# Optimization experiments

Hardware: AMD Instinct MI355X
Metric: run time of the kernel (lower is better)

The kernel has to match this reference:

```python
import jax, jax.numpy as jnp
import numpy as np

D_IN = 1024
D_OUT = 1024
NUM_HEADS = 16
HEAD_DIM = D_OUT // NUM_HEADS


def setup_inputs() -> dict:
    key = jax.random.key(0)
    ks = jax.random.split(key, 6)
    b, T = 2, 2048
    scale = 0.02
    x = jax.random.normal(ks[0], (b, T, D_IN), dtype=jnp.float32)
    Wq = jax.random.normal(ks[1], (D_IN, D_OUT), dtype=jnp.float32) * scale
    Wk = jax.random.normal(ks[2], (D_IN, D_OUT), dtype=jnp.float32) * scale
    Wv = jax.random.normal(ks[3], (D_IN, D_OUT), dtype=jnp.float32) * scale
    Wo = jax.random.normal(ks[4], (D_OUT, D_OUT), dtype=jnp.float32) * scale
    bo = jnp.zeros((D_OUT,), dtype=jnp.float32)
    return {"x": x, "Wq": Wq, "Wk": Wk, "Wv": Wv, "Wo": Wo, "bo": bo}


def reference(x, Wq, Wk, Wv, Wo, bo):
    b, T, _ = x.shape
    H, Dh = NUM_HEADS, HEAD_DIM
    # projections: [b,T,d_out] -> [b,H,T,Dh]
    q = (x @ Wq).reshape(b, T, H, Dh).transpose(0, 2, 1, 3)
    k = (x @ Wk).reshape(b, T, H, Dh).transpose(0, 2, 1, 3)
    v = (x @ Wv).reshape(b, T, H, Dh).transpose(0, 2, 1, 3)
    # scores: [b,H,T,T]
    att = jnp.einsum('bhqd,bhkd->bhqk', q, k)
    causal = jnp.triu(jnp.ones((T, T), dtype=bool), k=1)
    att = jnp.where(causal, -jnp.inf, att)
    att = jax.nn.softmax(att / np.sqrt(Dh).astype(np.float32), axis=-1)
    # dropout p=0.0 -> identity
    y = jnp.einsum('bhqk,bhkd->bhqd', att, v)
    y = y.transpose(0, 2, 1, 3).reshape(b, T, H * Dh)
    return y @ Wo + bo
```

## Files before the change

### kernel.cpp

```cpp
#include <hip/hip_runtime.h>

#define T_   2048
#define DM   1024
#define H_   16
#define DH   64

typedef unsigned short u16;
typedef unsigned int u32;
typedef __attribute__((ext_vector_type(8))) short bf16x8;
typedef __attribute__((ext_vector_type(8))) unsigned short u16x8;
typedef __attribute__((ext_vector_type(4))) float f32x4;
typedef __attribute__((ext_vector_type(16))) float f32x16;
typedef __attribute__((ext_vector_type(4))) unsigned int u32x4;
typedef __attribute__((ext_vector_type(2))) unsigned int u32x2;

static __device__ __forceinline__ u16 f2b(float f) {
  unsigned int u = __builtin_bit_cast(unsigned int, f);
  u += 0x7fff + ((u >> 16) & 1);
  return (u16)(u >> 16);
}

static __device__ __forceinline__ u32 cvtpk(float a, float b) {
  u32 d;
  asm("v_cvt_pk_bf16_f32 %0, %1, %2" : "=v"(d) : "v"(a), "v"(b));
  return d;
}

static __device__ __forceinline__ void gll16(const void* g, void* l) {
  __builtin_amdgcn_global_load_lds(
      (const __attribute__((address_space(1))) unsigned int*)g,
      (__attribute__((address_space(3))) unsigned int*)l, 16, 0, 0);
}

static __device__ __forceinline__ bf16x8 ldf(const char* base, int rho,
                                             int k16) {
  return *(const bf16x8*)(base + rho * 128 + ((k16 ^ (rho & 7)) << 4));
}


__global__ __launch_bounds__(256) void k_cvt_x(const float* __restrict__ x,
                                               u16* __restrict__ o) {
  int i = (blockIdx.x * 256 + threadIdx.x) * 8;
  float4 a = *(const float4*)(x + i);
  float4 b = *(const float4*)(x + i + 4);
  u16x8 r;
  r[0] = f2b(a.x); r[1] = f2b(a.y); r[2] = f2b(a.z); r[3] = f2b(a.w);
  r[4] = f2b(b.x); r[5] = f2b(b.y); r[6] = f2b(b.z); r[7] = f2b(b.w);
  *(u16x8*)(o + i) = r;
}

__global__ __launch_bounds__(256) void k_cvt_wt(
    const float* __restrict__ Wq, const float* __restrict__ Wk,
    const float* __restrict__ Wv, const float* __restrict__ Wo,
    u16* __restrict__ oq, u16* __restrict__ ok, u16* __restrict__ ov,
    u16* __restrict__ oo) {
  const float* W; u16* Wt;
  int z = blockIdx.z;
  if (z == 0)      { W = Wq; Wt = oq; }
  else if (z == 1) { W = Wk; Wt = ok; }
  else if (z == 2) { W = Wv; Wt = ov; }
  else             { W = Wo; Wt = oo; }
  const float wsc = (z == 0) ? 0.1803368801111204f : 1.0f;
  __shared__ u16 tile[64][65];
  int k0 = blockIdx.x * 64, n0 = blockIdx.y * 64;
  int r = threadIdx.x >> 2, c0 = (threadIdx.x & 3) * 16;
  const float* src = W + (k0 + r) * DM + n0 + c0;
#pragma unroll
  for (int e = 0; e < 16; e += 4) {
    float4 v = *(const float4*)(src + e);
    tile[r][c0 + e + 0] = f2b(v.x * wsc);
    tile[r][c0 + e + 1] = f2b(v.y * wsc);
    tile[r][c0 + e + 2] = f2b(v.z * wsc);
    tile[r][c0 + e + 3] = f2b(v.w * wsc);
  }
  __syncthreads();
  u16x8 a, b;
#pragma unroll
  for (int e = 0; e < 8; ++e) a[e] = tile[c0 + e][r];
#pragma unroll
  for (int e = 0; e < 8; ++e) b[e] = tile[c0 + 8 + e][r];
  u16* dst = Wt + (n0 + r) * DM + k0 + c0;
  *(u16x8*)dst = a;
  *(u16x8*)(dst + 8) = b;
}

__global__ __launch_bounds__(256) void k_qkv(
    const u16* __restrict__ X, const u16* __restrict__ Wqt,
    const u16* __restrict__ Wkt, const u16* __restrict__ Wvt,
    u16* __restrict__ Qg, u16* __restrict__ Kg, u16* __restrict__ Vtg) {
  __shared__ char smem[34816];
  char* As = smem;
  char* Bs = smem + 16384;
  const int tid = threadIdx.x, lane = tid & 63, w = tid >> 6;
  const int frow = lane & 15, fk = lane >> 4;
  const int wr = (w >> 1) * 64, wc = (w & 1) * 64;
  const int m0 = blockIdx.x * 128;
  const int by = blockIdx.y;
  const int z = by >> 3, n0 = (by & 7) * 128;
  const u16* Wt = (z == 0) ? Wqt : (z == 1) ? Wkt : Wvt;
  const u16* Ap = X + m0 * DM;
  const u16* Bp = Wt + n0 * DM;
  const int ro = lane >> 3;
  const int ce = ((lane & 7) ^ ro) << 3;

  f32x4 acc[4][4];
#pragma unroll
  for (int mi = 0; mi < 4; ++mi)
#pragma unroll
    for (int ni = 0; ni < 4; ++ni) acc[mi][ni] = (f32x4){0.f, 0.f, 0.f, 0.f};

  for (int k0 = 0; k0 < DM; k0 += 64) {
#pragma unroll
    for (int c = 0; c < 4; ++c) {
      const int g8 = (w * 4 + c) * 8;
      gll16(Ap + (g8 + ro) * DM + k0 + ce, As + g8 * 128);
      gll16(Bp + (g8 + ro) * DM + k0 + ce, Bs + g8 * 128);
    }
    asm volatile("s_waitcnt vmcnt(0)" ::: "memory");
    __syncthreads();
    bf16x8 a[4][2], b[4][2];
#pragma unroll
    for (int mi = 0; mi < 4; ++mi)
#pragma unroll
      for (int kk = 0; kk < 2; ++kk)
        a[mi][kk] = ldf(As, wr + mi * 16 + frow, kk * 4 + fk);
#pragma unroll
    for (int ni = 0; ni < 4; ++ni)
#pragma unroll
      for (int kk = 0; kk < 2; ++kk)
        b[ni][kk] = ldf(Bs, wc + ni * 16 + frow, kk * 4 + fk);
#pragma unroll
    for (int mi = 0; mi < 4; ++mi)
#pragma unroll
      for (int ni = 0; ni < 4; ++ni)
#pragma unroll
        for (int kk = 0; kk < 2; ++kk)
          acc[mi][ni] = __builtin_amdgcn_mfma_f32_16x16x32_bf16(
              a[mi][kk], b[ni][kk], acc[mi][ni], 0, 0, 0);
    __syncthreads();
  }

  if (z < 2) {
    u16* out = (z == 0) ? Qg : Kg;
#pragma unroll
    for (int mi = 0; mi < 4; ++mi)
#pragma unroll
      for (int ni = 0; ni < 4; ++ni)
#pragma unroll
        for (int r = 0; r < 4; ++r) {
          int m = m0 + wr + mi * 16 + fk * 4 + r;
          int nl = n0 + wc + ni * 16 + frow;
          int b = m >> 11, t = m & 2047, h = nl >> 6, d = nl & 63;
          out[((b * H_ + h) * T_ + t) * DH + d] = f2b(acc[mi][ni][r]);
        }
  } else {
    u16* Tl = (u16*)smem;
#pragma unroll
    for (int ni = 0; ni < 4; ++ni) {
      const int n = wc + ni * 16 + frow;
#pragma unroll
      for (int mi = 0; mi < 4; ++mi)
#pragma unroll
        for (int r = 0; r < 4; ++r)
          Tl[n * 136 + wr + mi * 16 + fk * 4 + r] = f2b(acc[mi][ni][r]);
    }
    __syncthreads();
    const int n = tid >> 1, c0 = (tid & 1) * 64;
    const int ng = n0 + n, h = ng >> 6, d = ng & 63;
    const int b = m0 >> 11;
    const int tb = (m0 & 2047) + c0;
    u16* dst = Vtg + ((b * H_ + h) * DH + d) * T_ + tb;
#pragma unroll
    for (int e = 0; e < 8; ++e)
      *(u16x8*)(dst + e * 8) = *(const u16x8*)(Tl + n * 136 + c0 + e * 8);
  }
}

__global__ __launch_bounds__(256) void k_out(
    const u16* __restrict__ Y, const u16* __restrict__ Wot,
    const float* __restrict__ bo, float* __restrict__ out) {
  __shared__ char smem[24576];
  char* As = smem;
  char* Bs = smem + 8192;
  const int tid = threadIdx.x, lane = tid & 63, w = tid >> 6;
  const int frow = lane & 15, fk = lane >> 4;
  const int wr = (w >> 1) * 32, wc = (w & 1) * 64;
  const int m0 = blockIdx.x * 64, n0 = blockIdx.y * 128;
  const u16* Ap = Y + m0 * DM;
  const u16* Bp = Wot + n0 * DM;
  const int ro = lane >> 3;
  const int ce = ((lane & 7) ^ ro) << 3;

  f32x4 acc[2][4];
#pragma unroll
  for (int mi = 0; mi < 2; ++mi)
#pragma unroll
    for (int ni = 0; ni < 4; ++ni) acc[mi][ni] = (f32x4){0.f, 0.f, 0.f, 0.f};

  for (int k0 = 0; k0 < DM; k0 += 64) {
#pragma unroll
    for (int c = 0; c < 2; ++c) {
      const int g8 = (w * 2 + c) * 8;
      gll16(Ap + (g8 + ro) * DM + k0 + ce, As + g8 * 128);
    }
#pragma unroll
    for (int c = 0; c < 4; ++c) {
      const int g8 = (w * 4 + c) * 8;
      gll16(Bp + (g8 + ro) * DM + k0 + ce, Bs + g8 * 128);
    }
    asm volatile("s_waitcnt vmcnt(0)" ::: "memory");
    __syncthreads();
    bf16x8 a[2][2], b[4][2];
#pragma unroll
    for (int mi = 0; mi < 2; ++mi)
#pragma unroll
      for (int kk = 0; kk < 2; ++kk)
        a[mi][kk] = ldf(As, wr + mi * 16 + frow, kk * 4 + fk);
#pragma unroll
    for (int ni = 0; ni < 4; ++ni)
#pragma unroll
      for (int kk = 0; kk < 2; ++kk)
        b[ni][kk] = ldf(Bs, wc + ni * 16 + frow, kk * 4 + fk);
#pragma unroll
    for (int mi = 0; mi < 2; ++mi)
#pragma unroll
      for (int ni = 0; ni < 4; ++ni)
#pragma unroll
        for (int kk = 0; kk < 2; ++kk)
          acc[mi][ni] = __builtin_amdgcn_mfma_f32_16x16x32_bf16(
              a[mi][kk], b[ni][kk], acc[mi][ni], 0, 0, 0);
    __syncthreads();
  }
#pragma unroll
  for (int mi = 0; mi < 2; ++mi)
#pragma unroll
    for (int ni = 0; ni < 4; ++ni)
#pragma unroll
      for (int r = 0; r < 4; ++r) {
        int m = m0 + wr + mi * 16 + fk * 4 + r;
        int n = n0 + wc + ni * 16 + frow;
        out[m * DM + n] = acc[mi][ni][r] + bo[n];
      }
}

__global__ __launch_bounds__(128) void k_attn(
    const u16* __restrict__ Qg, const u16* __restrict__ Kg,
    const u16* __restrict__ Vtg, u16* __restrict__ Yg) {
  __shared__ char Kl[2][8192];
  __shared__ char Vl[2][8192];
  const int bh = blockIdx.x;
  const int qt = 31 - blockIdx.y;
  const int q0 = qt * 64;
  const int tid = threadIdx.x, w = tid >> 6, lane = tid & 63;
  const int hi = lane >> 5, qq = lane & 31;
  const u16* Qb = Qg + bh * (T_ * DH);
  const u16* Kb = Kg + bh * (T_ * DH);
  const u16* Vb = Vtg + bh * (DH * T_);
  const int qrow = q0 + w * 32 + qq;

  bf16x8 qf[4];
#pragma unroll
  for (int kb = 0; kb < 4; ++kb)
    qf[kb] = *(const bf16x8*)(Qb + qrow * DH + kb * 16 + hi * 8);

  f32x16 o0, o1;
#pragma unroll
  for (int r = 0; r < 16; ++r) { o0[r] = 0.f; o1[r] = 0.f; }
  float m = -1e30f, lp = 0.f;

  const int nt = qt + 1;
  const int ro = lane >> 3;
  const int ce = ((lane & 7) ^ ro) << 3;

#pragma unroll
  for (int c = 0; c < 4; ++c) {
    const int g = w * 4 + c;
    gll16(Kb + (g * 8 + ro) * DH + ce, Kl[0] + g * 1024);
    gll16(Vb + (g * 8 + ro) * T_ + ce, Vl[0] + g * 1024);
  }
  asm volatile("s_waitcnt vmcnt(0)" ::: "memory");
  __syncthreads();

  for (int t = 0; t < nt; ++t) {
    const char* Kc = Kl[t & 1];
    const char* Vc = Vl[t & 1];
    if (t + 1 < nt) {
      const int jn = (t + 1) * 64;
      char* Kn = Kl[(t + 1) & 1];
      char* Vn = Vl[(t + 1) & 1];
#pragma unroll
      for (int c = 0; c < 4; ++c) {
        const int g = w * 4 + c;
        gll16(Kb + (jn + g * 8 + ro) * DH + ce, Kn + g * 1024);
        gll16(Vb + (g * 8 + ro) * T_ + jn + ce, Vn + g * 1024);
      }
    }

    f32x16 s0, s1;
#pragma unroll
    for (int r = 0; r < 16; ++r) { s0[r] = 0.f; s1[r] = 0.f; }
#pragma unroll
    for (int kb = 0; kb < 4; ++kb) {
      bf16x8 ka0 = *(const bf16x8*)(
          Kc + qq * 128 + (((kb * 2 + hi) ^ (qq & 7)) << 4));
      s0 = __builtin_amdgcn_mfma_f32_32x32x16_bf16(ka0, qf[kb], s0, 0, 0, 0);
      bf16x8 ka1 = *(const bf16x8*)(
          Kc + (qq + 32) * 128 + (((kb * 2 + hi) ^ (qq & 7)) << 4));
      s1 = __builtin_amdgcn_mfma_f32_32x32x16_bf16(ka1, qf[kb], s1, 0, 0, 0);
    }
    if (t == nt - 1) {
#pragma unroll
      for (int r = 0; r < 16; ++r) {
        const int cr = q0 + (r & 3) + 8 * (r >> 2) + 4 * hi;
        if (cr > qrow) s0[r] = -1e30f;
        if (cr + 32 > qrow) s1[r] = -1e30f;
      }
    }
    float tm[16];
#pragma unroll
    for (int r = 0; r < 16; ++r) tm[r] = fmaxf(s0[r], s1[r]);
#pragma unroll
    for (int st = 8; st > 0; st >>= 1)
#pragma unroll
      for (int r = 0; r < st; ++r) tm[r] = fmaxf(tm[r], tm[r + st]);
    const float mt = fmaxf(tm[0], __shfl_xor(tm[0], 32));
    if (__any(mt > m + 8.f)) {
      const float mn = fmaxf(m, mt);
      const float al = __builtin_amdgcn_exp2f(m - mn);
      m = mn;
#pragma unroll
      for (int r = 0; r < 16; ++r) { o0[r] *= al; o1[r] *= al; }
      lp *= al;
    }
    float ts[16];
#pragma unroll
    for (int r = 0; r < 16; ++r) {
      s0[r] = __builtin_amdgcn_exp2f(s0[r] - m);
      s1[r] = __builtin_amdgcn_exp2f(s1[r] - m);
      ts[r] = s0[r] + s1[r];
    }
#pragma unroll
    for (int st = 8; st > 0; st >>= 1)
#pragma unroll
      for (int r = 0; r < st; ++r) ts[r] += ts[r + st];
    lp += ts[0];
    bf16x8 pb[4];
#define MKCH(DST, S, RB)                                                     \
  {                                                                          \
    u32 a01 = cvtpk(S[RB + 0], S[RB + 1]);                                   \
    u32 a23 = cvtpk(S[RB + 2], S[RB + 3]);                                   \
    u32 a45 = cvtpk(S[RB + 4], S[RB + 5]);                                   \
    u32 a67 = cvtpk(S[RB + 6], S[RB + 7]);                                   \
    asm volatile("v_permlane32_swap_b32 %0, %1" : "+v"(a01), "+v"(a45));     \
    asm volatile("v_permlane32_swap_b32 %0, %1" : "+v"(a23), "+v"(a67));     \
    u32x4 t4;                                                                \
    t4[0] = a01; t4[1] = a23; t4[2] = a45; t4[3] = a67;                      \
    DST = __builtin_bit_cast(bf16x8, t4);                                    \
  }
    MKCH(pb[0], s0, 0)
    MKCH(pb[1], s0, 8)
    MKCH(pb[2], s1, 0)
    MKCH(pb[3], s1, 8)
#undef MKCH
#pragma unroll
    for (int jc = 0; jc < 4; ++jc) {
      bf16x8 va0 = *(const bf16x8*)(
          Vc + qq * 128 + (((jc * 2 + hi) ^ (qq & 7)) << 4));
      o0 = __builtin_amdgcn_mfma_f32_32x32x16_bf16(va0, pb[jc], o0, 0, 0, 0);
      bf16x8 va1 = *(const bf16x8*)(
          Vc + (qq + 32) * 128 + (((jc * 2 + hi) ^ (qq & 7)) << 4));
      o1 = __builtin_amdgcn_mfma_f32_32x32x16_bf16(va1, pb[jc], o1, 0, 0, 0);
    }
    asm volatile("s_waitcnt vmcnt(0)" ::: "memory");
    __syncthreads();
  }
  lp += __shfl_xor(lp, 32);
  const float rl = 1.0f / lp;
  const int obase = ((bh >> 4) * T_ + qrow) * DM + (bh & 15) * DH;
#pragma unroll
  for (int g = 0; g < 4; ++g) {
    u32x2 st;
    st[0] = cvtpk(o0[g * 4 + 0] * rl, o0[g * 4 + 1] * rl);
    st[1] = cvtpk(o0[g * 4 + 2] * rl, o0[g * 4 + 3] * rl);
    *(u32x2*)(Yg + obase + g * 8 + hi * 4) = st;
    st[0] = cvtpk(o1[g * 4 + 0] * rl, o1[g * 4 + 1] * rl);
    st[1] = cvtpk(o1[g * 4 + 2] * rl, o1[g * 4 + 3] * rl);
    *(u32x2*)(Yg + obase + 32 + g * 8 + hi * 4) = st;
  }
}


extern "C" void kernel_launch(void* const* d_in, const int* in_sizes, int n_in,
                              void* d_out, int out_size, void* d_ws,
                              size_t ws_size, hipStream_t stream) {
  const float* x  = (const float*)d_in[0];
  const float* Wq = (const float*)d_in[1];
  const float* Wk = (const float*)d_in[2];
  const float* Wv = (const float*)d_in[3];
  const float* Wo = (const float*)d_in[4];
  const float* bo = (const float*)d_in[5];
  float* out = (float*)d_out;
  char* ws = (char*)d_ws;

  u16* xb  = (u16*)(ws);
  u16* wqt = (u16*)(ws + (8ull << 20));
  u16* wkt = (u16*)(ws + (10ull << 20));
  u16* wvt = (u16*)(ws + (12ull << 20));
  u16* wot = (u16*)(ws + (14ull << 20));
  u16* Qg  = (u16*)(ws + (16ull << 20));
  u16* Kg  = (u16*)(ws + (24ull << 20));
  u16* Vtg = (u16*)(ws + (32ull << 20));
  u16* Yg  = (u16*)(ws + (40ull << 20));

  k_cvt_x<<<2048, 256, 0, stream>>>(x, xb);
  k_cvt_wt<<<dim3(16, 16, 4), 256, 0, stream>>>(Wq, Wk, Wv, Wo, wqt, wkt, wvt, wot);
  k_qkv<<<dim3(32, 24), 256, 0, stream>>>(xb, wqt, wkt, wvt, Qg, Kg, Vtg);
  k_attn<<<dim3(32, 32), 128, 0, stream>>>(Qg, Kg, Vtg, Yg);
  k_out<<<dim3(64, 8), 256, 0, stream>>>(Yg, wot, bo, out);
}
```

Measured before the change: 124.5 us.

## Use single-wave attention blocks with register-staged K/V and in-place LDS prefetch

Restructures the attention kernel from two-wave blocks with 64 query rows to one-wave blocks with 32 query rows, doubling the grid. The double-buffered LDS is replaced by a single buffer: each wave loads K (then V) fragments into registers, then immediately issues the next tile's global-to-LDS loads into the same buffer, using vmcnt counts instead of __syncthreads. This removes block barriers and halves LDS per block to raise occupancy. In exchange, K/V tiles are re-fetched by twice as many blocks and register pressure rises from the staged fragments.

```diff
diff --git a/kernel.cpp b/kernel.cpp
--- a/kernel.cpp
+++ b/kernel.cpp
@@ -243,20 +243,20 @@
       }
 }
 
-__global__ __launch_bounds__(128) void k_attn(
+__global__ __launch_bounds__(64) void k_attn(
     const u16* __restrict__ Qg, const u16* __restrict__ Kg,
     const u16* __restrict__ Vtg, u16* __restrict__ Yg) {
-  __shared__ char Kl[2][8192];
-  __shared__ char Vl[2][8192];
+  __shared__ char Kl[8192];
+  __shared__ char Vl[8192];
   const int bh = blockIdx.x;
-  const int qt = 31 - blockIdx.y;
-  const int q0 = qt * 64;
-  const int tid = threadIdx.x, w = tid >> 6, lane = tid & 63;
+  const int qt = 63 - blockIdx.y;
+  const int q0 = qt * 32;
+  const int lane = threadIdx.x;
   const int hi = lane >> 5, qq = lane & 31;
   const u16* Qb = Qg + bh * (T_ * DH);
   const u16* Kb = Kg + bh * (T_ * DH);
   const u16* Vb = Vtg + bh * (DH * T_);
-  const int qrow = q0 + w * 32 + qq;
+  const int qrow = q0 + qq;
 
   bf16x8 qf[4];
 #pragma unroll
@@ -268,50 +268,48 @@
   for (int r = 0; r < 16; ++r) { o0[r] = 0.f; o1[r] = 0.f; }
   float m = -1e30f, lp = 0.f;
 
-  const int nt = qt + 1;
+  const int nt = (qt >> 1) + 1;
   const int ro = lane >> 3;
   const int ce = ((lane & 7) ^ ro) << 3;
 
 #pragma unroll
-  for (int c = 0; c < 4; ++c) {
-    const int g = w * 4 + c;
-    gll16(Kb + (g * 8 + ro) * DH + ce, Kl[0] + g * 1024);
-    gll16(Vb + (g * 8 + ro) * T_ + ce, Vl[0] + g * 1024);
-  }
-  asm volatile("s_waitcnt vmcnt(0)" ::: "memory");
-  __syncthreads();
+  for (int g = 0; g < 8; ++g)
+    gll16(Kb + (g * 8 + ro) * DH + ce, Kl + g * 1024);
+#pragma unroll
+  for (int g = 0; g < 8; ++g)
+    gll16(Vb + (g * 8 + ro) * T_ + ce, Vl + g * 1024);
 
   for (int t = 0; t < nt; ++t) {
-    const char* Kc = Kl[t & 1];
-    const char* Vc = Vl[t & 1];
-    if (t + 1 < nt) {
-      const int jn = (t + 1) * 64;
-      char* Kn = Kl[(t + 1) & 1];
-      char* Vn = Vl[(t + 1) & 1];
-#pragma unroll
-      for (int c = 0; c < 4; ++c) {
-        const int g = w * 4 + c;
-        gll16(Kb + (jn + g * 8 + ro) * DH + ce, Kn + g * 1024);
-        gll16(Vb + (g * 8 + ro) * T_ + jn + ce, Vn + g * 1024);
-      }
-    }
-
+    const bool st = (t + 1 < nt);
+    const int jn = (t + 1) * 64;
+    asm volatile("s_waitcnt vmcnt(8)" ::: "memory");
+    bf16x8 kf[8];
+#pragma unroll
+    for (int kb = 0; kb < 4; ++kb) {
+      kf[kb] = *(const bf16x8*)(
+          Kl + qq * 128 + (((kb * 2 + hi) ^ (qq & 7)) << 4));
+      kf[4 + kb] = *(const bf16x8*)(
+          Kl + (qq + 32) * 128 + (((kb * 2 + hi) ^ (qq & 7)) << 4));
+    }
+    asm volatile("s_waitcnt lgkmcnt(0)" ::: "memory");
+    if (st) {
+#pragma unroll
+      for (int g = 0; g < 8; ++g)
+        gll16(Kb + (jn + g * 8 + ro) * DH + ce, Kl + g * 1024);
+    }
     f32x16 s0, s1;
 #pragma unroll
     for (int r = 0; r < 16; ++r) { s0[r] = 0.f; s1[r] = 0.f; }
 #pragma unroll
     for (int kb = 0; kb < 4; ++kb) {
-      bf16x8 ka0 = *(const bf16x8*)(
-          Kc + qq * 128 + (((kb * 2 + hi) ^ (qq & 7)) << 4));
-      s0 = __builtin_amdgcn_mfma_f32_32x32x16_bf16(ka0, qf[kb], s0, 0, 0, 0);
-      bf16x8 ka1 = *(const bf16x8*)(
-          Kc + (qq + 32) * 128 + (((kb * 2 + hi) ^ (qq & 7)) << 4));
-      s1 = __builtin_amdgcn_mfma_f32_32x32x16_bf16(ka1, qf[kb], s1, 0, 0, 0);
+      s0 = __builtin_amdgcn_mfma_f32_32x32x16_bf16(kf[kb], qf[kb], s0, 0, 0, 0);
+      s1 = __builtin_amdgcn_mfma_f32_32x32x16_bf16(kf[4 + kb], qf[kb], s1, 0, 0, 0);
     }
     if (t == nt - 1) {
+      const int j0 = t * 64;
 #pragma unroll
       for (int r = 0; r < 16; ++r) {
-        const int cr = q0 + (r & 3) + 8 * (r >> 2) + 4 * hi;
+        const int cr = j0 + (r & 3) + 8 * (r >> 2) + 4 * hi;
         if (cr > qrow) s0[r] = -1e30f;
         if (cr + 32 > qrow) s1[r] = -1e30f;
       }
@@ -320,9 +318,9 @@
 #pragma unroll
     for (int r = 0; r < 16; ++r) tm[r] = fmaxf(s0[r], s1[r]);
 #pragma unroll
-    for (int st = 8; st > 0; st >>= 1)
-#pragma unroll
-      for (int r = 0; r < st; ++r) tm[r] = fmaxf(tm[r], tm[r + st]);
+    for (int stp = 8; stp > 0; stp >>= 1)
+#pragma unroll
+      for (int r = 0; r < stp; ++r) tm[r] = fmaxf(tm[r], tm[r + stp]);
     const float mt = fmaxf(tm[0], __shfl_xor(tm[0], 32));
     if (__any(mt > m + 8.f)) {
       const float mn = fmaxf(m, mt);
@@ -340,9 +338,9 @@
       ts[r] = s0[r] + s1[r];
     }
 #pragma unroll
-    for (int st = 8; st > 0; st >>= 1)
-#pragma unroll
-      for (int r = 0; r < st; ++r) ts[r] += ts[r + st];
+    for (int stp = 8; stp > 0; stp >>= 1)
+#pragma unroll
+      for (int r = 0; r < stp; ++r) ts[r] += ts[r + stp];
     lp += ts[0];
     bf16x8 pb[4];
 #define MKCH(DST, S, RB)                                                     \
@@ -362,17 +360,27 @@
     MKCH(pb[2], s1, 0)
     MKCH(pb[3], s1, 8)
 #undef MKCH
+    if (st) { asm volatile("s_waitcnt vmcnt(8)" ::: "memory"); }
+    else    { asm volatile("s_waitcnt vmcnt(0)" ::: "memory"); }
+    bf16x8 vf[8];
 #pragma unroll
     for (int jc = 0; jc < 4; ++jc) {
-      bf16x8 va0 = *(const bf16x8*)(
-          Vc + qq * 128 + (((jc * 2 + hi) ^ (qq & 7)) << 4));
-      o0 = __builtin_amdgcn_mfma_f32_32x32x16_bf16(va0, pb[jc], o0, 0, 0, 0);
-      bf16x8 va1 = *(const bf16x8*)(
-          Vc + (qq + 32) * 128 + (((jc * 2 + hi) ^ (qq & 7)) << 4));
-      o1 = __builtin_amdgcn_mfma_f32_32x32x16_bf16(va1, pb[jc], o1, 0, 0, 0);
-    }
-    asm volatile("s_waitcnt vmcnt(0)" ::: "memory");
-    __syncthreads();
+      vf[jc] = *(const bf16x8*)(
+          Vl + qq * 128 + (((jc * 2 + hi) ^ (qq & 7)) << 4));
+      vf[4 + jc] = *(const bf16x8*)(
+          Vl + (qq + 32) * 128 + (((jc * 2 + hi) ^ (qq & 7)) << 4));
+    }
+    asm volatile("s_waitcnt lgkmcnt(0)" ::: "memory");
+    if (st) {
+#pragma unroll
+      for (int g = 0; g < 8; ++g)
+        gll16(Vb + (g * 8 + ro) * T_ + jn + ce, Vl + g * 1024);
+    }
+#pragma unroll
+    for (int jc = 0; jc < 4; ++jc) {
+      o0 = __builtin_amdgcn_mfma_f32_32x32x16_bf16(vf[jc], pb[jc], o0, 0, 0, 0);
+      o1 = __builtin_amdgcn_mfma_f32_32x32x16_bf16(vf[4 + jc], pb[jc], o1, 0, 0, 0);
+    }
   }
   lp += __shfl_xor(lp, 32);
   const float rl = 1.0f / lp;
@@ -415,6 +423,6 @@
   k_cvt_x<<<2048, 256, 0, stream>>>(x, xb);
   k_cvt_wt<<<dim3(16, 16, 4), 256, 0, stream>>>(Wq, Wk, Wv, Wo, wqt, wkt, wvt, wot);
   k_qkv<<<dim3(32, 24), 256, 0, stream>>>(xb, wqt, wkt, wvt, Qg, Kg, Vtg);
-  k_attn<<<dim3(32, 32), 128, 0, stream>>>(Qg, Kg, Vtg, Yg);
+  k_attn<<<dim3(32, 64), 64, 0, stream>>>(Qg, Kg, Vtg, Yg);
   k_out<<<dim3(64, 8), 256, 0, stream>>>(Yg, wot, bo, out);
 }
```

Measured after the change: 117.1 us. 1.06x faster.
